# Kernel tuning notes

Hardware: AMD Instinct MI355X
Metric: run time of the kernel (lower is better)

The kernel has to match this reference:

```python
import jax, jax.numpy as jnp
import numpy as np

N_NODES = 100000
N_EDGES = 1600000
VOCAB = 15000
D_IN = 128
D_HID = 128
N_GRAPHS = 16


def setup_inputs() -> dict:
    key = jax.random.key(0)
    ks = jax.random.split(key, 16)
    stdv = 1.0 / np.sqrt(D_HID)
    inp = {
        "word_ids": jax.random.randint(ks[0], (N_NODES,), 0, VOCAB),
        "edge_src": jax.random.randint(ks[1], (N_EDGES,), 0, N_NODES),
        "edge_dst": jax.random.randint(ks[2], (N_EDGES,), 0, N_NODES),
        "edge_weight": jax.random.uniform(ks[3], (N_EDGES,), dtype=jnp.float32),
        "norm": jax.random.uniform(ks[4], (N_NODES,), dtype=jnp.float32),
        "graph_id": jnp.sort(jax.random.randint(ks[5], (N_NODES,), 0, N_GRAPHS)),
        "y_data": jax.random.uniform(ks[6], (N_GRAPHS,), dtype=jnp.float32),
        # learned params
        "word_embeds": jax.random.normal(ks[7], (VOCAB, D_IN), dtype=jnp.float32) * 0.05,
        "W0": jax.random.uniform(ks[8], (D_IN, D_HID), minval=-stdv, maxval=stdv, dtype=jnp.float32),
        "b0": jax.random.uniform(ks[9], (D_HID,), minval=-stdv, maxval=stdv, dtype=jnp.float32),
        "W1": jax.random.uniform(ks[10], (D_HID, D_HID), minval=-stdv, maxval=stdv, dtype=jnp.float32),
        "b1": jax.random.uniform(ks[11], (D_HID,), minval=-stdv, maxval=stdv, dtype=jnp.float32),
        "Wout": jax.random.uniform(ks[12], (D_HID, 1), minval=-stdv, maxval=stdv, dtype=jnp.float32),
        "bout": jax.random.uniform(ks[13], (1,), minval=-stdv, maxval=stdv, dtype=jnp.float32),
    }
    return inp


def _gcn_layer(h, W, b, norm, edge_src, edge_dst, edge_weight):
    # h: [N, d_in] -> [N, d_out]
    h = h @ W                                   # dense projection
    h = h * norm[:, None]                       # pre-aggregation norm
    msg = h[edge_src] * edge_weight[:, None]    # u_mul_e   [E, d]
    h = jax.ops.segment_sum(msg, edge_dst, num_segments=N_NODES)  # sum agg
    h = h * norm[:, None]                       # post-aggregation norm
    return jax.nn.relu(h + b)


def reference(word_ids, edge_src, edge_dst, edge_weight, norm, graph_id, y_data,
              word_embeds, W0, b0, W1, b1, Wout, bout):
    h = word_embeds[word_ids]                   # [N, D_IN]
    h = _gcn_layer(h, W0, b0, norm, edge_src, edge_dst, edge_weight)
    h = _gcn_layer(h, W1, b1, norm, edge_src, edge_dst, edge_weight)
    # per-graph max pooling (dgl.max_nodes)
    g = jax.ops.segment_max(h, graph_id, num_segments=N_GRAPHS)   # [B, D_HID]
    z = g @ Wout + bout                          # [B, 1] logits
    zf = z.reshape(-1)
    # binary_cross_entropy_with_logits, mean reduction (numerically stable)
    loss = jnp.mean(jnp.maximum(zf, 0.0) - zf * y_data + jnp.log1p(jnp.exp(-jnp.abs(zf))))
    y_pred = jax.nn.sigmoid(z)
    return loss, y_pred
```

## Files before the change

kernel.cpp:

```cpp
#include <hip/hip_runtime.h>
#include <math.h>

#define D 128
#define NG 16
#define NBINS 512
#define CHUNK 2048
#define CAPB 4608

typedef unsigned int uint;
typedef unsigned short ushort;
typedef unsigned long long u64;
typedef __attribute__((ext_vector_type(8))) short bf16x8;
typedef __attribute__((ext_vector_type(4))) float f32x4;

__device__ __forceinline__ ushort f32_to_bf16(float f) {
    uint b = __float_as_uint(f);
    b += 0x7fffu + ((b >> 16) & 1u);
    return (ushort)(b >> 16);
}
__device__ __forceinline__ uint pack_bf16x2(float lo, float hi) {
    return (uint)f32_to_bf16(lo) | ((uint)f32_to_bf16(hi) << 16);
}
__device__ __forceinline__ float sb(uint u) {
    return (float)(int)(signed char)(u & 0xffu);
}

__global__ __launch_bounds__(256) void k_binA(
    const int* __restrict__ esrc, const int* __restrict__ edst,
    const float* __restrict__ ew, const float* __restrict__ norm,
    u64* __restrict__ binned, int* __restrict__ loc_off,
    int* __restrict__ bin_cnt, int ne, int width)
{
    __shared__ int hist[NBINS], lscan[NBINS], lcur[NBINS];
    __shared__ int ws4[4];
    __shared__ u64 stage[CHUNK];
    const int tid = threadIdx.x;
    const int base = blockIdx.x * CHUNK;
    const int count = min(CHUNK, ne - base);

    hist[tid] = 0; hist[tid + 256] = 0;
    __syncthreads();

    int s[8], bn[8], dl[8]; float c[8];
    #pragma unroll
    for (int i = 0; i < 8; ++i) {
        int li = i * 256 + tid;
        bn[i] = -1;
        if (li < count) {
            int e = base + li;
            s[i] = esrc[e];
            int d = edst[e];
            bn[i] = d / width;
            dl[i] = d - bn[i] * width;
            c[i] = ew[e] * norm[s[i]];
            atomicAdd(&hist[bn[i]], 1);
        }
    }
    __syncthreads();

    {
        int lane = tid & 63, w = tid >> 6;
        int h0 = hist[2 * tid], h1 = hist[2 * tid + 1];
        int sum = h0 + h1, x = sum;
        for (int dlt = 1; dlt < 64; dlt <<= 1) {
            int t2 = __shfl_up(x, dlt);
            if (lane >= dlt) x += t2;
        }
        if (lane == 63) ws4[w] = x;
        __syncthreads();
        if (tid == 0) { int run = 0; for (int i = 0; i < 4; ++i) { int t3 = ws4[i]; ws4[i] = run; run += t3; } }
        __syncthreads();
        int b0 = ws4[w] + (x - sum);
        lscan[2 * tid] = b0;       lscan[2 * tid + 1] = b0 + h0;
        lcur[2 * tid] = b0;        lcur[2 * tid + 1] = b0 + h0;
    }
    __syncthreads();

    int* lo = loc_off + (size_t)blockIdx.x * (NBINS + 1);
    lo[tid] = lscan[tid]; lo[tid + 256] = lscan[tid + 256];
    if (tid == 0) lo[NBINS] = count;
    if (hist[tid])       atomicAdd(&bin_cnt[tid], hist[tid]);
    if (hist[tid + 256]) atomicAdd(&bin_cnt[tid + 256], hist[tid + 256]);

    #pragma unroll
    for (int i = 0; i < 8; ++i) {
        if (bn[i] >= 0) {
            int pos = atomicAdd(&lcur[bn[i]], 1);
            uint packed = (uint)s[i] | ((uint)dl[i] << 24);
            stage[pos] = ((u64)__float_as_uint(c[i]) << 32) | packed;
        }
    }
    __syncthreads();

    u64* outp = binned + (size_t)blockIdx.x * CHUNK;
    for (int j = tid; j < count; j += 256) outp[j] = stage[j];
}

__global__ __launch_bounds__(1024) void k_scan_top(int* __restrict__ bsum, int nb)
{
    int tid = threadIdx.x, lane = tid & 63, w = tid >> 6;
    int v = tid < nb ? bsum[tid] : 0;
    int x = v;
    for (int d = 1; d < 64; d <<= 1) {
        int t = __shfl_up(x, d);
        if (lane >= d) x += t;
    }
    __shared__ int ws[16];
    if (lane == 63) ws[w] = x;
    __syncthreads();
    if (tid == 0) { int run = 0; for (int i = 0; i < 16; ++i) { int t = ws[i]; ws[i] = run; run += t; } }
    __syncthreads();
    x += ws[w];
    if (tid < nb) bsum[tid] = x - v;
}

__global__ __launch_bounds__(256) void k_binB(
    const u64* __restrict__ binned, const int* __restrict__ loc_off,
    const int* __restrict__ bin_off, int* __restrict__ off,
    int2* __restrict__ csr, int n, int ne, int width, int nA)
{
    __shared__ u64 stA[CAPB];
    __shared__ int hist[256], cur[256];
    __shared__ int wsum[4];
    __shared__ int sTotal;
    const int tid = threadIdx.x;
    const int bin = blockIdx.x;
    const int d0 = bin * width;
    const int dcount = min(n - d0, width);
    const int base = bin_off[bin];

    if (tid == 0) sTotal = 0;
    hist[tid] = 0;
    __syncthreads();

    if (dcount > 0) {
        for (int f = tid; f < nA; f += 256) {
            const int* lo = loc_off + (size_t)f * (NBINS + 1);
            int a = lo[bin], b = lo[bin + 1];
            int len = b - a;
            if (len > 0) {
                int st = atomicAdd(&sTotal, len);
                const u64* src = binned + (size_t)f * CHUNK + a;
                for (int k = 0; k < len; ++k) {
                    u64 r = src[k];
                    stA[st + k] = r;
                    atomicAdd(&hist[(int)((r >> 24) & 0xFF)], 1);
                }
            }
        }
    }
    __syncthreads();
    const int cnt = sTotal;

    {
        int lane = tid & 63, w = tid >> 6;
        int v = hist[tid], x = v;
        for (int dlt = 1; dlt < 64; dlt <<= 1) {
            int t2 = __shfl_up(x, dlt);
            if (lane >= dlt) x += t2;
        }
        if (lane == 63) wsum[w] = x;
        __syncthreads();
        if (tid == 0) { int run = 0; for (int i = 0; i < 4; ++i) { int t3 = wsum[i]; wsum[i] = run; run += t3; } }
        __syncthreads();
        int ex = wsum[w] + x - v;
        cur[tid] = ex;
        if (tid < dcount) off[d0 + tid] = base + ex;
    }
    if (tid == 0 && dcount > 0 && d0 + dcount == n) off[n] = base + cnt;
    __syncthreads();

    for (int i = tid; i < cnt; i += 256) {
        u64 r = stA[i];
        int dl = (int)((r >> 24) & 0xFF);
        int pos = atomicAdd(&cur[dl], 1);
        csr[base + pos] = make_int2((int)(r & 0xFFFFFF), (int)(r >> 32));
    }
}

__global__ __launch_bounds__(256) void k_wfrag(
    const float* __restrict__ W, ushort* __restrict__ Wf)
{
    int t = blockIdx.x * 256 + threadIdx.x;
    if (t >= 2048) return;
    int lane = t & 63, tile = t >> 6;
    int ks = tile & 3, nt = tile >> 2;
    int col = nt * 16 + (lane & 15);
    int k0 = ks * 32 + (lane >> 4) * 8;
    ushort* dst = Wf + (size_t)t * 8;
    #pragma unroll
    for (int j = 0; j < 8; ++j)
        dst[j] = f32_to_bf16(W[(k0 + j) * D + col]);
}

__global__ __launch_bounds__(256) void k_proj(
    const float* __restrict__ emb, const ushort* __restrict__ Wf,
    ushort* __restrict__ P, int vocab)
{
    int lane = threadIdx.x & 63;
    int w = threadIdx.x >> 6;
    int rowbase = blockIdx.x * 64 + w * 16;
    int arow = rowbase + (lane & 15);
    const bf16x8* WfV = reinterpret_cast<const bf16x8*>(Wf);
    f32x4 acc[8] = {};
    #pragma unroll
    for (int ks = 0; ks < 4; ++ks) {
        bf16x8 af = {0, 0, 0, 0, 0, 0, 0, 0};
        if (arow < vocab) {
            int k0 = ks * 32 + (lane >> 4) * 8;
            float4 a0 = *reinterpret_cast<const float4*>(emb + (size_t)arow * D + k0);
            float4 a1 = *reinterpret_cast<const float4*>(emb + (size_t)arow * D + k0 + 4);
            af[0] = (short)f32_to_bf16(a0.x); af[1] = (short)f32_to_bf16(a0.y);
            af[2] = (short)f32_to_bf16(a0.z); af[3] = (short)f32_to_bf16(a0.w);
            af[4] = (short)f32_to_bf16(a1.x); af[5] = (short)f32_to_bf16(a1.y);
            af[6] = (short)f32_to_bf16(a1.z); af[7] = (short)f32_to_bf16(a1.w);
        }
        #pragma unroll
        for (int nt = 0; nt < 8; ++nt) {
            bf16x8 bf = WfV[(nt * 4 + ks) * 64 + lane];
            acc[nt] = __builtin_amdgcn_mfma_f32_16x16x32_bf16(af, bf, acc[nt], 0, 0, 0);
        }
    }
    int r0 = rowbase + (lane >> 4) * 4;
    #pragma unroll
    for (int nt = 0; nt < 8; ++nt) {
        int col = nt * 16 + (lane & 15);
        #pragma unroll
        for (int i = 0; i < 4; ++i) {
            int r = r0 + i;
            if (r < vocab) P[(size_t)r * D + col] = f32_to_bf16(acc[nt][i]);
        }
    }
}

__global__ __launch_bounds__(256) void k_agg_proj(
    const int* __restrict__ off, const int2* __restrict__ csr,
    const int* __restrict__ wid, const ushort* __restrict__ P,
    const float* __restrict__ norm, const float* __restrict__ bias,
    char* __restrict__ out8, float* __restrict__ scale, int n)
{
    int row = blockIdx.x * 8 + (threadIdx.x >> 5);
    if (row >= n) return;
    int q = threadIdx.x & 31;
    int h = q >> 4;
    int c8 = (q & 15) * 8;
    int j0 = off[row], j1 = off[row + 1];
    float acc[8] = {0.f, 0.f, 0.f, 0.f, 0.f, 0.f, 0.f, 0.f};

    for (int jb = j0; jb < j1; jb += 32) {
        int m = min(32, j1 - jb);
        int2 p = make_int2(0, 0);
        if (q < m) {
            p = csr[jb + q];
            p.x = wid[p.x];
        }
        int t = 0;
        for (; t + 8 <= m; t += 8) {
            uint4 u[4]; float wv[4];
            #pragma unroll
            for (int k = 0; k < 4; ++k) {
                int eh = t + 2 * k + h;
                int sv = __shfl(p.x, eh, 32);
                wv[k] = __int_as_float(__shfl(p.y, eh, 32));
                u[k] = *reinterpret_cast<const uint4*>(P + (size_t)sv * D + c8);
            }
            #pragma unroll
            for (int k = 0; k < 4; ++k) {
                acc[0] = fmaf(__uint_as_float(u[k].x << 16),          wv[k], acc[0]);
                acc[1] = fmaf(__uint_as_float(u[k].x & 0xffff0000u),  wv[k], acc[1]);
                acc[2] = fmaf(__uint_as_float(u[k].y << 16),          wv[k], acc[2]);
                acc[3] = fmaf(__uint_as_float(u[k].y & 0xffff0000u),  wv[k], acc[3]);
                acc[4] = fmaf(__uint_as_float(u[k].z << 16),          wv[k], acc[4]);
                acc[5] = fmaf(__uint_as_float(u[k].z & 0xffff0000u),  wv[k], acc[5]);
                acc[6] = fmaf(__uint_as_float(u[k].w << 16),          wv[k], acc[6]);
                acc[7] = fmaf(__uint_as_float(u[k].w & 0xffff0000u),  wv[k], acc[7]);
            }
        }
        for (; t < m; t += 2) {
            int eh = t + h;
            int sv = __shfl(p.x, eh, 32);
            float wvv = __int_as_float(__shfl(p.y, eh, 32));
            uint4 u = *reinterpret_cast<const uint4*>(P + (size_t)sv * D + c8);
            acc[0] = fmaf(__uint_as_float(u.x << 16),         wvv, acc[0]);
            acc[1] = fmaf(__uint_as_float(u.x & 0xffff0000u), wvv, acc[1]);
            acc[2] = fmaf(__uint_as_float(u.y << 16),         wvv, acc[2]);
            acc[3] = fmaf(__uint_as_float(u.y & 0xffff0000u), wvv, acc[3]);
            acc[4] = fmaf(__uint_as_float(u.z << 16),         wvv, acc[4]);
            acc[5] = fmaf(__uint_as_float(u.z & 0xffff0000u), wvv, acc[5]);
            acc[6] = fmaf(__uint_as_float(u.w << 16),         wvv, acc[6]);
            acc[7] = fmaf(__uint_as_float(u.w & 0xffff0000u), wvv, acc[7]);
        }
    }
    #pragma unroll
    for (int i = 0; i < 8; ++i) acc[i] += __shfl_xor(acc[i], 16, 32);

    float nm = norm[row];
    float4 bv0 = *reinterpret_cast<const float4*>(bias + c8);
    float4 bv1 = *reinterpret_cast<const float4*>(bias + c8 + 4);
    float v[8];
    v[0] = fmaxf(fmaf(acc[0], nm, bv0.x), 0.f);
    v[1] = fmaxf(fmaf(acc[1], nm, bv0.y), 0.f);
    v[2] = fmaxf(fmaf(acc[2], nm, bv0.z), 0.f);
    v[3] = fmaxf(fmaf(acc[3], nm, bv0.w), 0.f);
    v[4] = fmaxf(fmaf(acc[4], nm, bv1.x), 0.f);
    v[5] = fmaxf(fmaf(acc[5], nm, bv1.y), 0.f);
    v[6] = fmaxf(fmaf(acc[6], nm, bv1.z), 0.f);
    v[7] = fmaxf(fmaf(acc[7], nm, bv1.w), 0.f);
    float mx = v[0];
    #pragma unroll
    for (int i = 1; i < 8; ++i) mx = fmaxf(mx, v[i]);
    #pragma unroll
    for (int d = 1; d < 16; d <<= 1) mx = fmaxf(mx, __shfl_xor(mx, d, 32));

    float inv = (mx > 0.f) ? 127.f / mx : 0.f;
    if (q == 0) scale[row] = (mx > 0.f) ? mx * (1.f / 127.f) : 0.f;
    if (h == 0) {
        uint b0 = 0, b1 = 0;
        #pragma unroll
        for (int i = 0; i < 4; ++i) {
            int qv = min(__float2int_rn(v[i] * inv), 127);
            b0 |= ((uint)qv & 0xffu) << (8 * i);
        }
        #pragma unroll
        for (int i = 0; i < 4; ++i) {
            int qv = min(__float2int_rn(v[4 + i] * inv), 127);
            b1 |= ((uint)qv & 0xffu) << (8 * i);
        }
        *reinterpret_cast<uint2*>(out8 + (size_t)row * D + c8) = make_uint2(b0, b1);
    }
}

__global__ __launch_bounds__(256) void k_agg_q8(
    const int* __restrict__ off, const int2* __restrict__ csr,
    const char* __restrict__ tab8, const float* __restrict__ scale,
    ushort* __restrict__ outbf, int n)
{
    int row = blockIdx.x * 8 + (threadIdx.x >> 5);
    if (row >= n) return;
    int q = threadIdx.x & 31;
    int h = q >> 4;
    int c8 = (q & 15) * 8;
    int j0 = off[row], j1 = off[row + 1];
    float acc[8] = {0.f, 0.f, 0.f, 0.f, 0.f, 0.f, 0.f, 0.f};

    for (int jb = j0; jb < j1; jb += 32) {
        int m = min(32, j1 - jb);
        int2 p = make_int2(0, 0);
        if (q < m) p = csr[jb + q];
        int t = 0;
        for (; t + 8 <= m; t += 8) {
            uint2 u[4]; float wv[4];
            #pragma unroll
            for (int k = 0; k < 4; ++k) {
                int eh = t + 2 * k + h;
                int sv = __shfl(p.x, eh, 32);
                float wc = __int_as_float(__shfl(p.y, eh, 32));
                wv[k] = wc * scale[sv];
                u[k] = *reinterpret_cast<const uint2*>(tab8 + (size_t)sv * D + c8);
            }
            #pragma unroll
            for (int k = 0; k < 4; ++k) {
                acc[0] = fmaf(sb(u[k].x),       wv[k], acc[0]);
                acc[1] = fmaf(sb(u[k].x >> 8),  wv[k], acc[1]);
                acc[2] = fmaf(sb(u[k].x >> 16), wv[k], acc[2]);
                acc[3] = fmaf(sb(u[k].x >> 24), wv[k], acc[3]);
                acc[4] = fmaf(sb(u[k].y),       wv[k], acc[4]);
                acc[5] = fmaf(sb(u[k].y >> 8),  wv[k], acc[5]);
                acc[6] = fmaf(sb(u[k].y >> 16), wv[k], acc[6]);
                acc[7] = fmaf(sb(u[k].y >> 24), wv[k], acc[7]);
            }
        }
        for (; t < m; t += 2) {
            int eh = t + h;
            int sv = __shfl(p.x, eh, 32);
            float wc = __int_as_float(__shfl(p.y, eh, 32));
            float wvv = wc * scale[sv];
            uint2 u = *reinterpret_cast<const uint2*>(tab8 + (size_t)sv * D + c8);
            acc[0] = fmaf(sb(u.x),       wvv, acc[0]);
            acc[1] = fmaf(sb(u.x >> 8),  wvv, acc[1]);
            acc[2] = fmaf(sb(u.x >> 16), wvv, acc[2]);
            acc[3] = fmaf(sb(u.x >> 24), wvv, acc[3]);
            acc[4] = fmaf(sb(u.y),       wvv, acc[4]);
            acc[5] = fmaf(sb(u.y >> 8),  wvv, acc[5]);
            acc[6] = fmaf(sb(u.y >> 16), wvv, acc[6]);
            acc[7] = fmaf(sb(u.y >> 24), wvv, acc[7]);
        }
    }
    #pragma unroll
    for (int i = 0; i < 8; ++i) acc[i] += __shfl_xor(acc[i], 16, 32);
    if (h == 0) {
        uint4 o;
        o.x = pack_bf16x2(acc[0], acc[1]);
        o.y = pack_bf16x2(acc[2], acc[3]);
        o.z = pack_bf16x2(acc[4], acc[5]);
        o.w = pack_bf16x2(acc[6], acc[7]);
        *reinterpret_cast<uint4*>(outbf + (size_t)row * D + c8) = o;
    }
}

__device__ __forceinline__ void gemm_core_16x128(
    const ushort* __restrict__ aggbf, const ushort* __restrict__ Wf,
    int rowbase, int lane, int n, f32x4 acc[8])
{
    int arow = rowbase + (lane & 15);
    const bf16x8* WfV = reinterpret_cast<const bf16x8*>(Wf);
    #pragma unroll
    for (int ks = 0; ks < 4; ++ks) {
        bf16x8 af = {0, 0, 0, 0, 0, 0, 0, 0};
        if (arow < n) {
            int k0 = ks * 32 + (lane >> 4) * 8;
            af = *reinterpret_cast<const bf16x8*>(aggbf + (size_t)arow * D + k0);
        }
        #pragma unroll
        for (int nt = 0; nt < 8; ++nt) {
            bf16x8 bf = WfV[(nt * 4 + ks) * 64 + lane];
            acc[nt] = __builtin_amdgcn_mfma_f32_16x16x32_bf16(af, bf, acc[nt], 0, 0, 0);
        }
    }
}

__global__ __launch_bounds__(256) void k_gemm_mfma_segmax(
    const ushort* __restrict__ aggbf, const ushort* __restrict__ Wf,
    const float* __restrict__ norm, const float* __restrict__ b,
    const int* __restrict__ gid, unsigned* __restrict__ g, int n)
{
    __shared__ float sh[64][132];
    __shared__ int sgid[64];
    int lane = threadIdx.x & 63;
    int w = threadIdx.x >> 6;
    int rowbase = blockIdx.x * 64 + w * 16;
    f32x4 acc[8] = {};
    gemm_core_16x128(aggbf, Wf, rowbase, lane, n, acc);

    int r0 = rowbase + (lane >> 4) * 4;
    int lr0 = w * 16 + (lane >> 4) * 4;
    float nrm[4];
    #pragma unroll
    for (int i = 0; i < 4; ++i) nrm[i] = (r0 + i < n) ? norm[r0 + i] : 0.f;
    #pragma unroll
    for (int nt = 0; nt < 8; ++nt) {
        int col = nt * 16 + (lane & 15);
        float bc = b[col];
        #pragma unroll
        for (int i = 0; i < 4; ++i) {
            float v = (r0 + i < n) ? fmaxf(fmaf(acc[nt][i], nrm[i], bc), 0.f) : 0.f;
            sh[lr0 + i][col] = v;
        }
    }
    if (threadIdx.x < 64) {
        int r = blockIdx.x * 64 + threadIdx.x;
        sgid[threadIdx.x] = (r < n) ? gid[r] : -1;
    }
    __syncthreads();

    if (threadIdx.x < D) {
        int c = threadIdx.x;
        int glo = 0x7fffffff, ghi = -1;
        #pragma unroll
        for (int i = 0; i < 64; ++i) {
            int gv = sgid[i];
            if (gv >= 0) { glo = min(glo, gv); ghi = max(ghi, gv); }
        }
        for (int gr = glo; gr <= ghi; ++gr) {
            float m = 0.f;
            #pragma unroll
            for (int i = 0; i < 64; ++i)
                if (sgid[i] == gr) m = fmaxf(m, sh[i][c]);
            if (m > 0.f) atomicMax(&g[gr * D + c], __float_as_uint(m));
        }
    }
}

__global__ __launch_bounds__(1024) void k_final(
    const unsigned* __restrict__ g, const float* __restrict__ Wout,
    const float* __restrict__ bout, const float* __restrict__ y,
    float* __restrict__ out)
{
    __shared__ float zs[NG];
    int wave = threadIdx.x >> 6, lane = threadIdx.x & 63;
    float acc = 0.f;
    for (int c = lane; c < D; c += 64)
        acc += __uint_as_float(g[wave * D + c]) * Wout[c];
    for (int off2 = 32; off2; off2 >>= 1) acc += __shfl_down(acc, off2);
    if (lane == 0) {
        float z = acc + bout[0];
        zs[wave] = z;
        out[1 + wave] = 1.f / (1.f + expf(-z));
    }
    __syncthreads();
    if (threadIdx.x == 0) {
        float loss = 0.f;
        for (int i = 0; i < NG; ++i) {
            float z = zs[i];
            loss += fmaxf(z, 0.f) - z * y[i] + log1pf(expf(-fabsf(z)));
        }
        out[0] = loss / NG;
    }
}

extern "C" void kernel_launch(void* const* d_in, const int* in_sizes, int n_in,
                              void* d_out, int out_size, void* d_ws, size_t ws_size,
                              hipStream_t stream) {
    const int*   word_ids = (const int*)  d_in[0];
    const int*   esrc     = (const int*)  d_in[1];
    const int*   edst     = (const int*)  d_in[2];
    const float* ew       = (const float*)d_in[3];
    const float* norm     = (const float*)d_in[4];
    const int*   gid      = (const int*)  d_in[5];
    const float* y        = (const float*)d_in[6];
    const float* embeds   = (const float*)d_in[7];
    const float* W0       = (const float*)d_in[8];
    const float* b0       = (const float*)d_in[9];
    const float* W1       = (const float*)d_in[10];
    const float* b1       = (const float*)d_in[11];
    const float* Wout     = (const float*)d_in[12];
    const float* bout     = (const float*)d_in[13];

    const int n  = in_sizes[0];
    const int ne = in_sizes[1];
    const int vocab = in_sizes[7] / D;
    float* out = (float*)d_out;

    const int nA = (ne + CHUNK - 1) / CHUNK;
    const int width = (n + NBINS - 1) / NBINS;

    ushort* aggbf = (ushort*)d_ws;
    int*    off   = (int*)(aggbf + (size_t)n * D);
    int*    bcnt  = off + (n + 1);
    int*    loff  = bcnt + NBINS;
    uintptr_t bin_addr = ((uintptr_t)(loff + (size_t)nA * (NBINS + 1)) + 15) & ~(uintptr_t)15;
    u64*    binned = (u64*)bin_addr;
    int2*   csr   = (int2*)(binned + (size_t)nA * CHUNK);
    char*   h1q   = (char*)(csr + ne);
    float*  hscale = (float*)(h1q + (size_t)n * D);
    uintptr_t p_addr = ((uintptr_t)(hscale + n) + 15) & ~(uintptr_t)15;
    ushort* P     = (ushort*)p_addr;
    unsigned* g   = (unsigned*)(P + (size_t)vocab * D);
    uintptr_t wf_addr = ((uintptr_t)(g + NG * D) + 15) & ~(uintptr_t)15;
    ushort* w0f = (ushort*)wf_addr;
    ushort* w1f = w0f + D * D;

    const dim3 blk(256);
    const int ablocks = (n + 7) / 8;
    const int mblocks = (n + 63) / 64;
    const int pblocks = (vocab + 63) / 64;

    hipMemsetAsync(bcnt, 0, NBINS * sizeof(int), stream);
    k_binA<<<nA, blk, 0, stream>>>(esrc, edst, ew, norm, binned, loff, bcnt, ne, width);
    k_scan_top<<<1, 1024, 0, stream>>>(bcnt, NBINS);
    k_binB<<<NBINS, blk, 0, stream>>>(binned, loff, bcnt, off, csr, n, ne, width, nA);

    k_wfrag<<<8, blk, 0, stream>>>(W0, w0f);
    k_wfrag<<<8, blk, 0, stream>>>(W1, w1f);
    k_proj<<<pblocks, blk, 0, stream>>>(embeds, w0f, P, vocab);

    k_agg_proj<<<ablocks, blk, 0, stream>>>(off, csr, word_ids, P, norm, b0, h1q, hscale, n);

    k_agg_q8<<<ablocks, blk, 0, stream>>>(off, csr, h1q, hscale, aggbf, n);
    hipMemsetAsync(g, 0, NG * D * sizeof(unsigned), stream);
    k_gemm_mfma_segmax<<<mblocks, blk, 0, stream>>>(aggbf, w1f, norm, b1, gid, g, n);

    k_final<<<1, 1024, 0, stream>>>(g, Wout, bout, y, out);
}
```

Before: 216.0 us.

## Quantize projected embedding table to int8 and widen aggregation to 16 columns per lane

The projected embedding table P is now stored as int8 with a per-row scale instead of bf16, which halves the bytes gathered per edge in the first aggregation. Both aggregation kernels now have each lane process 16 int8 columns through 16-byte loads, so one 32-lane group handles 4 edges at a time. The per-source scale is folded into the edge weight once when the CSR chunk is loaded, rather than being reloaded for every gathered row. In exchange, layer 1 takes on additional int8 quantization error, and each lane now holds 16 accumulators and needs an extra shuffle-reduction step.

```diff
diff --git a/kernel.cpp b/kernel.cpp
--- a/kernel.cpp
+++ b/kernel.cpp
@@ -23,6 +23,24 @@
 }
 __device__ __forceinline__ float sb(uint u) {
     return (float)(int)(signed char)(u & 0xffu);
+}
+__device__ __forceinline__ void fma16_i8(uint4 u, float w, float* acc) {
+    acc[0]  = fmaf(sb(u.x),       w, acc[0]);
+    acc[1]  = fmaf(sb(u.x >> 8),  w, acc[1]);
+    acc[2]  = fmaf(sb(u.x >> 16), w, acc[2]);
+    acc[3]  = fmaf(sb(u.x >> 24), w, acc[3]);
+    acc[4]  = fmaf(sb(u.y),       w, acc[4]);
+    acc[5]  = fmaf(sb(u.y >> 8),  w, acc[5]);
+    acc[6]  = fmaf(sb(u.y >> 16), w, acc[6]);
+    acc[7]  = fmaf(sb(u.y >> 24), w, acc[7]);
+    acc[8]  = fmaf(sb(u.z),       w, acc[8]);
+    acc[9]  = fmaf(sb(u.z >> 8),  w, acc[9]);
+    acc[10] = fmaf(sb(u.z >> 16), w, acc[10]);
+    acc[11] = fmaf(sb(u.z >> 24), w, acc[11]);
+    acc[12] = fmaf(sb(u.w),       w, acc[12]);
+    acc[13] = fmaf(sb(u.w >> 8),  w, acc[13]);
+    acc[14] = fmaf(sb(u.w >> 16), w, acc[14]);
+    acc[15] = fmaf(sb(u.w >> 24), w, acc[15]);
 }
 
 __global__ __launch_bounds__(256) void k_binA(
@@ -195,7 +213,7 @@
 
 __global__ __launch_bounds__(256) void k_proj(
     const float* __restrict__ emb, const ushort* __restrict__ Wf,
-    ushort* __restrict__ P, int vocab)
+    char* __restrict__ P8, float* __restrict__ pscale, int vocab)
 {
     int lane = threadIdx.x & 63;
     int w = threadIdx.x >> 6;
@@ -222,111 +240,115 @@
         }
     }
     int r0 = rowbase + (lane >> 4) * 4;
+    float mx[4] = {0.f, 0.f, 0.f, 0.f};
+    #pragma unroll
+    for (int nt = 0; nt < 8; ++nt)
+        #pragma unroll
+        for (int i = 0; i < 4; ++i) mx[i] = fmaxf(mx[i], fabsf(acc[nt][i]));
+    #pragma unroll
+    for (int d = 1; d < 16; d <<= 1)
+        #pragma unroll
+        for (int i = 0; i < 4; ++i) mx[i] = fmaxf(mx[i], __shfl_xor(mx[i], d, 64));
+    float inv[4];
+    #pragma unroll
+    for (int i = 0; i < 4; ++i) inv[i] = (mx[i] > 0.f) ? 127.f / mx[i] : 0.f;
+    if ((lane & 15) == 0) {
+        #pragma unroll
+        for (int i = 0; i < 4; ++i)
+            if (r0 + i < vocab) pscale[r0 + i] = (mx[i] > 0.f) ? mx[i] * (1.f / 127.f) : 0.f;
+    }
     #pragma unroll
     for (int nt = 0; nt < 8; ++nt) {
         int col = nt * 16 + (lane & 15);
         #pragma unroll
         for (int i = 0; i < 4; ++i) {
             int r = r0 + i;
-            if (r < vocab) P[(size_t)r * D + col] = f32_to_bf16(acc[nt][i]);
+            if (r < vocab) {
+                int qv = __float2int_rn(acc[nt][i] * inv[i]);
+                qv = max(-127, min(127, qv));
+                P8[(size_t)r * D + col] = (char)qv;
+            }
         }
     }
 }
 
 __global__ __launch_bounds__(256) void k_agg_proj(
     const int* __restrict__ off, const int2* __restrict__ csr,
-    const int* __restrict__ wid, const ushort* __restrict__ P,
-    const float* __restrict__ norm, const float* __restrict__ bias,
-    char* __restrict__ out8, float* __restrict__ scale, int n)
+    const int* __restrict__ wid, const char* __restrict__ P8,
+    const float* __restrict__ pscale, const float* __restrict__ norm,
+    const float* __restrict__ bias, char* __restrict__ out8,
+    float* __restrict__ scale, int n)
 {
     int row = blockIdx.x * 8 + (threadIdx.x >> 5);
     if (row >= n) return;
     int q = threadIdx.x & 31;
-    int h = q >> 4;
-    int c8 = (q & 15) * 8;
+    int e4 = q >> 3;
+    int c16 = (q & 7) * 16;
     int j0 = off[row], j1 = off[row + 1];
-    float acc[8] = {0.f, 0.f, 0.f, 0.f, 0.f, 0.f, 0.f, 0.f};
+    float acc[16] = {};
 
     for (int jb = j0; jb < j1; jb += 32) {
         int m = min(32, j1 - jb);
         int2 p = make_int2(0, 0);
         if (q < m) {
             p = csr[jb + q];
-            p.x = wid[p.x];
+            int wv_ = wid[p.x];
+            p.y = __float_as_int(__int_as_float(p.y) * pscale[wv_]);
+            p.x = wv_;
         }
         int t = 0;
-        for (; t + 8 <= m; t += 8) {
+        for (; t + 16 <= m; t += 16) {
             uint4 u[4]; float wv[4];
             #pragma unroll
             for (int k = 0; k < 4; ++k) {
-                int eh = t + 2 * k + h;
+                int eh = t + 4 * k + e4;
                 int sv = __shfl(p.x, eh, 32);
                 wv[k] = __int_as_float(__shfl(p.y, eh, 32));
-                u[k] = *reinterpret_cast<const uint4*>(P + (size_t)sv * D + c8);
+                u[k] = *reinterpret_cast<const uint4*>(P8 + (size_t)sv * D + c16);
             }
             #pragma unroll
-            for (int k = 0; k < 4; ++k) {
-                acc[0] = fmaf(__uint_as_float(u[k].x << 16),          wv[k], acc[0]);
-                acc[1] = fmaf(__uint_as_float(u[k].x & 0xffff0000u),  wv[k], acc[1]);
-                acc[2] = fmaf(__uint_as_float(u[k].y << 16),          wv[k], acc[2]);
-                acc[3] = fmaf(__uint_as_float(u[k].y & 0xffff0000u),  wv[k], acc[3]);
-                acc[4] = fmaf(__uint_as_float(u[k].z << 16),          wv[k], acc[4]);
-                acc[5] = fmaf(__uint_as_float(u[k].z & 0xffff0000u),  wv[k], acc[5]);
-                acc[6] = fmaf(__uint_as_float(u[k].w << 16),          wv[k], acc[6]);
-                acc[7] = fmaf(__uint_as_float(u[k].w & 0xffff0000u),  wv[k], acc[7]);
-            }
-        }
-        for (; t < m; t += 2) {
-            int eh = t + h;
-            int sv = __shfl(p.x, eh, 32);
-            float wvv = __int_as_float(__shfl(p.y, eh, 32));
-            uint4 u = *reinterpret_cast<const uint4*>(P + (size_t)sv * D + c8);
-            acc[0] = fmaf(__uint_as_float(u.x << 16),         wvv, acc[0]);
-            acc[1] = fmaf(__uint_as_float(u.x & 0xffff0000u), wvv, acc[1]);
-            acc[2] = fmaf(__uint_as_float(u.y << 16),         wvv, acc[2]);
-            acc[3] = fmaf(__uint_as_float(u.y & 0xffff0000u), wvv, acc[3]);
-            acc[4] = fmaf(__uint_as_float(u.z << 16),         wvv, acc[4]);
-            acc[5] = fmaf(__uint_as_float(u.z & 0xffff0000u), wvv, acc[5]);
-            acc[6] = fmaf(__uint_as_float(u.w << 16),         wvv, acc[6]);
-            acc[7] = fmaf(__uint_as_float(u.w & 0xffff0000u), wvv, acc[7]);
-        }
-    }
-    #pragma unroll
-    for (int i = 0; i < 8; ++i) acc[i] += __shfl_xor(acc[i], 16, 32);
-
+            for (int k = 0; k < 4; ++k) fma16_i8(u[k], wv[k], acc);
+        }
+        for (; t < m; t += 4) {
+            int eh = t + e4;
+            int sv = __shfl(p.x, eh & 31, 32);
+            float wvv = __int_as_float(__shfl(p.y, eh & 31, 32));
+            if (eh >= m) wvv = 0.f;
+            uint4 u = *reinterpret_cast<const uint4*>(P8 + (size_t)sv * D + c16);
+            fma16_i8(u, wvv, acc);
+        }
+    }
+    #pragma unroll
+    for (int i = 0; i < 16; ++i) {
+        acc[i] += __shfl_xor(acc[i], 8, 32);
+        acc[i] += __shfl_xor(acc[i], 16, 32);
+    }
     float nm = norm[row];
-    float4 bv0 = *reinterpret_cast<const float4*>(bias + c8);
-    float4 bv1 = *reinterpret_cast<const float4*>(bias + c8 + 4);
-    float v[8];
-    v[0] = fmaxf(fmaf(acc[0], nm, bv0.x), 0.f);
-    v[1] = fmaxf(fmaf(acc[1], nm, bv0.y), 0.f);
-    v[2] = fmaxf(fmaf(acc[2], nm, bv0.z), 0.f);
-    v[3] = fmaxf(fmaf(acc[3], nm, bv0.w), 0.f);
-    v[4] = fmaxf(fmaf(acc[4], nm, bv1.x), 0.f);
-    v[5] = fmaxf(fmaf(acc[5], nm, bv1.y), 0.f);
-    v[6] = fmaxf(fmaf(acc[6], nm, bv1.z), 0.f);
-    v[7] = fmaxf(fmaf(acc[7], nm, bv1.w), 0.f);
+    float v[16];
+    #pragma unroll
+    for (int i = 0; i < 16; i += 4) {
+        float4 bv = *reinterpret_cast<const float4*>(bias + c16 + i);
+        v[i + 0] = fmaxf(fmaf(acc[i + 0], nm, bv.x), 0.f);
+        v[i + 1] = fmaxf(fmaf(acc[i + 1], nm, bv.y), 0.f);
+        v[i + 2] = fmaxf(fmaf(acc[i + 2], nm, bv.z), 0.f);
+        v[i + 3] = fmaxf(fmaf(acc[i + 3], nm, bv.w), 0.f);
+    }
     float mx = v[0];
     #pragma unroll
-    for (int i = 1; i < 8; ++i) mx = fmaxf(mx, v[i]);
-    #pragma unroll
-    for (int d = 1; d < 16; d <<= 1) mx = fmaxf(mx, __shfl_xor(mx, d, 32));
-
+    for (int i = 1; i < 16; ++i) mx = fmaxf(mx, v[i]);
+    #pragma unroll
+    for (int d = 1; d < 8; d <<= 1) mx = fmaxf(mx, __shfl_xor(mx, d, 32));
     float inv = (mx > 0.f) ? 127.f / mx : 0.f;
     if (q == 0) scale[row] = (mx > 0.f) ? mx * (1.f / 127.f) : 0.f;
-    if (h == 0) {
-        uint b0 = 0, b1 = 0;
-        #pragma unroll
-        for (int i = 0; i < 4; ++i) {
+    if (q < 8) {
+        uint b4[4] = {0, 0, 0, 0};
+        #pragma unroll
+        for (int i = 0; i < 16; ++i) {
             int qv = min(__float2int_rn(v[i] * inv), 127);
-            b0 |= ((uint)qv & 0xffu) << (8 * i);
-        }
-        #pragma unroll
-        for (int i = 0; i < 4; ++i) {
-            int qv = min(__float2int_rn(v[4 + i] * inv), 127);
-            b1 |= ((uint)qv & 0xffu) << (8 * i);
-        }
-        *reinterpret_cast<uint2*>(out8 + (size_t)row * D + c8) = make_uint2(b0, b1);
+            b4[i >> 2] |= ((uint)qv & 0xffu) << (8 * (i & 3));
+        }
+        *reinterpret_cast<uint4*>(out8 + (size_t)row * D + c16) =
+            make_uint4(b4[0], b4[1], b4[2], b4[3]);
     }
 }
 
@@ -338,63 +360,53 @@
     int row = blockIdx.x * 8 + (threadIdx.x >> 5);
     if (row >= n) return;
     int q = threadIdx.x & 31;
-    int h = q >> 4;
-    int c8 = (q & 15) * 8;
+    int e4 = q >> 3;
+    int c16 = (q & 7) * 16;
     int j0 = off[row], j1 = off[row + 1];
-    float acc[8] = {0.f, 0.f, 0.f, 0.f, 0.f, 0.f, 0.f, 0.f};
+    float acc[16] = {};
 
     for (int jb = j0; jb < j1; jb += 32) {
         int m = min(32, j1 - jb);
         int2 p = make_int2(0, 0);
-        if (q < m) p = csr[jb + q];
+        if (q < m) {
+            p = csr[jb + q];
+            p.y = __float_as_int(__int_as_float(p.y) * scale[p.x]);
+        }
         int t = 0;
-        for (; t + 8 <= m; t += 8) {
-            uint2 u[4]; float wv[4];
+        for (; t + 16 <= m; t += 16) {
+            uint4 u[4]; float wv[4];
             #pragma unroll
             for (int k = 0; k < 4; ++k) {
-                int eh = t + 2 * k + h;
+                int eh = t + 4 * k + e4;
                 int sv = __shfl(p.x, eh, 32);
-                float wc = __int_as_float(__shfl(p.y, eh, 32));
-                wv[k] = wc * scale[sv];
-                u[k] = *reinterpret_cast<const uint2*>(tab8 + (size_t)sv * D + c8);
+                wv[k] = __int_as_float(__shfl(p.y, eh, 32));
+                u[k] = *reinterpret_cast<const uint4*>(tab8 + (size_t)sv * D + c16);
             }
             #pragma unroll
-            for (int k = 0; k < 4; ++k) {
-                acc[0] = fmaf(sb(u[k].x),       wv[k], acc[0]);
-                acc[1] = fmaf(sb(u[k].x >> 8),  wv[k], acc[1]);
-                acc[2] = fmaf(sb(u[k].x >> 16), wv[k], acc[2]);
-                acc[3] = fmaf(sb(u[k].x >> 24), wv[k], acc[3]);
-                acc[4] = fmaf(sb(u[k].y),       wv[k], acc[4]);
-                acc[5] = fmaf(sb(u[k].y >> 8),  wv[k], acc[5]);
-                acc[6] = fmaf(sb(u[k].y >> 16), wv[k], acc[6]);
-                acc[7] = fmaf(sb(u[k].y >> 24), wv[k], acc[7]);
-            }
-        }
-        for (; t < m; t += 2) {
-            int eh = t + h;
-            int sv = __shfl(p.x, eh, 32);
-            float wc = __int_as_float(__shfl(p.y, eh, 32));
-            float wvv = wc * scale[sv];
-            uint2 u = *reinterpret_cast<const uint2*>(tab8 + (size_t)sv * D + c8);
-            acc[0] = fmaf(sb(u.x),       wvv, acc[0]);
-            acc[1] = fmaf(sb(u.x >> 8),  wvv, acc[1]);
-            acc[2] = fmaf(sb(u.x >> 16), wvv, acc[2]);
-            acc[3] = fmaf(sb(u.x >> 24), wvv, acc[3]);
-            acc[4] = fmaf(sb(u.y),       wvv, acc[4]);
-            acc[5] = fmaf(sb(u.y >> 8),  wvv, acc[5]);
-            acc[6] = fmaf(sb(u.y >> 16), wvv, acc[6]);
-            acc[7] = fmaf(sb(u.y >> 24), wvv, acc[7]);
-        }
-    }
-    #pragma unroll
-    for (int i = 0; i < 8; ++i) acc[i] += __shfl_xor(acc[i], 16, 32);
-    if (h == 0) {
-        uint4 o;
-        o.x = pack_bf16x2(acc[0], acc[1]);
-        o.y = pack_bf16x2(acc[2], acc[3]);
-        o.z = pack_bf16x2(acc[4], acc[5]);
-        o.w = pack_bf16x2(acc[6], acc[7]);
-        *reinterpret_cast<uint4*>(outbf + (size_t)row * D + c8) = o;
+            for (int k = 0; k < 4; ++k) fma16_i8(u[k], wv[k], acc);
+        }
+        for (; t < m; t += 4) {
+            int eh = t + e4;
+            int sv = __shfl(p.x, eh & 31, 32);
+            float wvv = __int_as_float(__shfl(p.y, eh & 31, 32));
+            if (eh >= m) wvv = 0.f;
+            uint4 u = *reinterpret_cast<const uint4*>(tab8 + (size_t)sv * D + c16);
+            fma16_i8(u, wvv, acc);
+        }
+    }
+    #pragma unroll
+    for (int i = 0; i < 16; ++i) {
+        acc[i] += __shfl_xor(acc[i], 8, 32);
+        acc[i] += __shfl_xor(acc[i], 16, 32);
+    }
+    if (q < 8) {
+        uint4 oA, oB;
+        oA.x = pack_bf16x2(acc[0], acc[1]);   oA.y = pack_bf16x2(acc[2], acc[3]);
+        oA.z = pack_bf16x2(acc[4], acc[5]);   oA.w = pack_bf16x2(acc[6], acc[7]);
+        oB.x = pack_bf16x2(acc[8], acc[9]);   oB.y = pack_bf16x2(acc[10], acc[11]);
+        oB.z = pack_bf16x2(acc[12], acc[13]); oB.w = pack_bf16x2(acc[14], acc[15]);
+        *reinterpret_cast<uint4*>(outbf + (size_t)row * D + c16) = oA;
+        *reinterpret_cast<uint4*>(outbf + (size_t)row * D + c16 + 8) = oB;
     }
 }
 
@@ -534,8 +546,9 @@
     char*   h1q   = (char*)(csr + ne);
     float*  hscale = (float*)(h1q + (size_t)n * D);
     uintptr_t p_addr = ((uintptr_t)(hscale + n) + 15) & ~(uintptr_t)15;
-    ushort* P     = (ushort*)p_addr;
-    unsigned* g   = (unsigned*)(P + (size_t)vocab * D);
+    char*   P8    = (char*)p_addr;
+    float*  pscale = (float*)(P8 + (size_t)vocab * D);
+    unsigned* g   = (unsigned*)(pscale + vocab);
     uintptr_t wf_addr = ((uintptr_t)(g + NG * D) + 15) & ~(uintptr_t)15;
     ushort* w0f = (ushort*)wf_addr;
     ushort* w1f = w0f + D * D;
@@ -552,9 +565,9 @@
 
     k_wfrag<<<8, blk, 0, stream>>>(W0, w0f);
     k_wfrag<<<8, blk, 0, stream>>>(W1, w1f);
-    k_proj<<<pblocks, blk, 0, stream>>>(embeds, w0f, P, vocab);
-
-    k_agg_proj<<<ablocks, blk, 0, stream>>>(off, csr, word_ids, P, norm, b0, h1q, hscale, n);
+    k_proj<<<pblocks, blk, 0, stream>>>(embeds, w0f, P8, pscale, vocab);
+
+    k_agg_proj<<<ablocks, blk, 0, stream>>>(off, csr, word_ids, P8, pscale, norm, b0, h1q, hscale, n);
 
     k_agg_q8<<<ablocks, blk, 0, stream>>>(off, csr, h1q, hscale, aggbf, n);
     hipMemsetAsync(g, 0, NG * D * sizeof(unsigned), stream);
```

After: 243.9 us. 12.9% more time.
